# Kernel optimization log

Hardware: AMD Instinct MI355X
Metric: run time of the kernel (lower is better)

Reference implementation:

```python
import jax, jax.numpy as jnp
import numpy as np

D_MODEL = 1024
NUM_HEADS = 16
D_K = D_MODEL // NUM_HEADS


def setup_inputs() -> dict:
    key = jax.random.key(0)
    ks = jax.random.split(key, 7)
    B, S = 2, 2048
    scale = 1.0 / np.sqrt(D_MODEL)
    return {
        "Q": jax.random.normal(ks[0], (B, S, D_MODEL), dtype=jnp.float32),
        "K": jax.random.normal(ks[1], (B, S, D_MODEL), dtype=jnp.float32),
        "V": jax.random.normal(ks[2], (B, S, D_MODEL), dtype=jnp.float32),
        "W_q": jax.random.normal(ks[3], (D_MODEL, D_MODEL), dtype=jnp.float32) * scale,
        "W_k": jax.random.normal(ks[4], (D_MODEL, D_MODEL), dtype=jnp.float32) * scale,
        "W_v": jax.random.normal(ks[5], (D_MODEL, D_MODEL), dtype=jnp.float32) * scale,
        "W_o": jax.random.normal(ks[6], (D_MODEL, D_MODEL), dtype=jnp.float32) * scale,
    }


def _split_heads(x):
    B, S, _ = x.shape
    return x.reshape(B, S, NUM_HEADS, D_K).transpose(0, 2, 1, 3)  # [B,H,S,Dk]


def reference(Q, K, V, W_q, W_k, W_v, W_o):
    # nn.Linear(bias=False): x @ W.T
    q = _split_heads(Q @ W_q.T)
    k = _split_heads(K @ W_k.T)
    v = _split_heads(V @ W_v.T)
    scores = jnp.einsum("bhqd,bhkd->bhqk", q, k) / jnp.sqrt(jnp.float32(D_K))
    probs = jax.nn.softmax(scores, axis=-1)
    out = jnp.einsum("bhqk,bhkd->bhqd", probs, v)  # [B,H,S,Dk]
    B, H, S, Dk = out.shape
    out = out.transpose(0, 2, 1, 3).reshape(B, S, H * Dk)
    return out @ W_o.T
```

## Files before the change

kernel.cpp:

```cpp
#include <hip/hip_runtime.h>
#include <cstdint>

#define D_MODEL 1024
#define NH 16
#define DK 64
#define SEQ 2048
#define BATCH 2
#define M_TOT (BATCH * SEQ)

typedef __bf16 bf16x8          __attribute__((ext_vector_type(8)));
typedef unsigned short u16x8   __attribute__((ext_vector_type(8)));
typedef float  f32x4           __attribute__((ext_vector_type(4)));

union pun8 { u16x8 u; bf16x8 b; };

__device__ __forceinline__ f32x4 mfma16(bf16x8 a, bf16x8 b, f32x4 c) {
    return __builtin_amdgcn_mfma_f32_16x16x32_bf16(a, b, c, 0, 0, 0);
}

__device__ __forceinline__ unsigned short f2bf(float f) {
    union { float f; uint32_t u; } v; v.f = f;
    uint32_t u = v.u;
    return (unsigned short)((u + 0x7FFFu + ((u >> 16) & 1u)) >> 16);
}

__device__ __forceinline__ unsigned short f2bf_trunc(float f) {
    union { float f; uint32_t u; } v; v.f = f;
    return (unsigned short)(v.u >> 16);
}

__device__ __forceinline__ void gl_lds16(const unsigned short* g, unsigned short* l) {
    __builtin_amdgcn_global_load_lds(
        (const __attribute__((address_space(1))) void*)g,
        (__attribute__((address_space(3))) void*)l, 16, 0, 0);
}

#define C_EXP2 0.1803368801111204f

__global__ __launch_bounds__(256) void convert_all_kernel(
    const float* __restrict__ Q,  const float* __restrict__ K,
    const float* __restrict__ V,  const float* __restrict__ Wq,
    const float* __restrict__ Wk, const float* __restrict__ Wv,
    const float* __restrict__ Wo,
    unsigned short* __restrict__ Qb,  unsigned short* __restrict__ Kb,
    unsigned short* __restrict__ Vb,  unsigned short* __restrict__ Wqb,
    unsigned short* __restrict__ Wkb, unsigned short* __restrict__ Wvb,
    unsigned short* __restrict__ Wob)
{
    int bid = blockIdx.x;
    const float* src; unsigned short* dst; int base;
    if (bid < 3 * 2048) {
        int r = bid >> 11;
        src  = (r == 0) ? Q  : (r == 1) ? K  : V;
        dst  = (r == 0) ? Qb : (r == 1) ? Kb : Vb;
        base = (bid & 2047) * 2048;
    } else {
        int u = bid - 3 * 2048;
        int r = u >> 9;
        src  = (r == 0) ? Wq  : (r == 1) ? Wk  : (r == 2) ? Wv  : Wo;
        dst  = (r == 0) ? Wqb : (r == 1) ? Wkb : (r == 2) ? Wvb : Wob;
        base = (u & 511) * 2048;
    }
    int i = base + threadIdx.x * 8;
    float4 a = *(const float4*)(src + i);
    float4 b = *(const float4*)(src + i + 4);
    u16x8 o;
    o[0] = f2bf(a.x); o[1] = f2bf(a.y); o[2] = f2bf(a.z); o[3] = f2bf(a.w);
    o[4] = f2bf(b.x); o[5] = f2bf(b.y); o[6] = f2bf(b.z); o[7] = f2bf(b.w);
    *(u16x8*)(dst + i) = o;
}

__global__ __launch_bounds__(256) void qkv_proj_kernel(
    const unsigned short* __restrict__ Q,
    const unsigned short* __restrict__ K,
    const unsigned short* __restrict__ V,
    const unsigned short* __restrict__ Wq,
    const unsigned short* __restrict__ Wk,
    const unsigned short* __restrict__ Wv,
    unsigned short* __restrict__ qb,
    unsigned short* __restrict__ kb,
    unsigned short* __restrict__ vtb)
{
    const int z = blockIdx.z;
    const unsigned short* A  = (z == 0) ? Q  : (z == 1) ? K  : V;
    const unsigned short* Bt = (z == 0) ? Wq : (z == 1) ? Wk : Wv;

    const int m0 = blockIdx.y * 128;
    const int n0 = blockIdx.x * 128;

    __shared__ __align__(16) unsigned short smem[128 * 136];
    unsigned short* As = smem;
    unsigned short* Bs = smem + 128 * 64;
    unsigned short* Cs = smem;

    const int t    = threadIdx.x;
    const int lane = t & 63;
    const int w    = t >> 6;
    const int l15  = lane & 15;
    const int quad = lane >> 4;
    const int wm   = (w >> 1) * 64;
    const int wn   = (w & 1) * 64;

    f32x4 acc[4][4] = {};

    for (int k0 = 0; k0 < D_MODEL; k0 += 64) {
        __syncthreads();
        #pragma unroll
        for (int i = 0; i < 4; i++) {
            int u   = t + i * 256;
            int row = u >> 3;
            int kc  = (u & 7) * 8;
            gl_lds16(&A [(m0 + row) * D_MODEL + k0 + kc], &As[(i * 256 + w * 64) * 8]);
            gl_lds16(&Bt[(n0 + row) * D_MODEL + k0 + kc], &Bs[(i * 256 + w * 64) * 8]);
        }
        __syncthreads();

        #pragma unroll
        for (int kk = 0; kk < 2; kk++) {
            bf16x8 a[4], b[4];
            #pragma unroll
            for (int mi = 0; mi < 4; mi++)
                a[mi] = *(const bf16x8*)(&As[(wm + mi * 16 + l15) * 64 + kk * 32 + quad * 8]);
            #pragma unroll
            for (int ni = 0; ni < 4; ni++)
                b[ni] = *(const bf16x8*)(&Bs[(wn + ni * 16 + l15) * 64 + kk * 32 + quad * 8]);

            #pragma unroll
            for (int mi = 0; mi < 4; mi++)
                #pragma unroll
                for (int ni = 0; ni < 4; ni++)
                    acc[mi][ni] = mfma16(a[mi], b[ni], acc[mi][ni]);
        }
    }

    const float oscale = (z == 0) ? C_EXP2 : 1.0f;
    __syncthreads();
    #pragma unroll
    for (int mi = 0; mi < 4; mi++) {
        #pragma unroll
        for (int ni = 0; ni < 4; ni++) {
            #pragma unroll
            for (int r = 0; r < 4; r++) {
                int rloc = wm + mi * 16 + quad * 4 + r;
                int cloc = wn + ni * 16 + l15;
                int rr = (z == 2) ? cloc : rloc;
                int cc = (z == 2) ? rloc : cloc;
                Cs[rr * 136 + cc] = f2bf(acc[mi][ni][r] * oscale);
            }
        }
    }
    __syncthreads();
    #pragma unroll
    for (int i = 0; i < 8; i++) {
        int u    = t + i * 256;
        int rrow = u >> 4;
        int cc8  = (u & 15) * 8;
        u16x8 val = *(const u16x8*)(&Cs[rrow * 136 + cc8]);
        unsigned short* dst;
        if (z < 2) {
            int m = m0 + rrow, n = n0 + cc8;
            int bi = m >> 11, s = m & (SEQ - 1);
            int hh = n >> 6,  d = n & (DK - 1);
            dst = ((z == 0) ? qb : kb) + (((size_t)(bi * NH + hh) * SEQ + s) * DK + d);
        } else {
            int dglob = n0 + rrow;
            int bi = m0 >> 11, s = (m0 & (SEQ - 1)) + cc8;
            int hh = dglob >> 6, d = dglob & (DK - 1);
            dst = vtb + (((size_t)(bi * NH + hh) * DK + d) * SEQ + s);
        }
        *(u16x8*)dst = val;
    }
}

__global__ __launch_bounds__(256) void attn_kernel(
    const unsigned short* __restrict__ qb,
    const unsigned short* __restrict__ kb,
    const unsigned short* __restrict__ vtb,
    unsigned short* __restrict__ ctx)
{
    const int h  = blockIdx.x;
    const int qt = blockIdx.y;
    const int b  = blockIdx.z;

    const int t    = threadIdx.x;
    const int lane = t & 63;
    const int w    = t >> 6;
    const int l15  = lane & 15;
    const int quad = lane >> 4;

    const unsigned short* qh = qb  + ((b * NH + h) * SEQ) * DK;
    const unsigned short* kh = kb  + ((b * NH + h) * SEQ) * DK;
    const unsigned short* vh = vtb + ((b * NH + h) * DK) * SEQ;

    __shared__ __align__(16) unsigned short p_lds[4][32][72];
    __shared__ __align__(16) unsigned short Ks[128 * 72];
    __shared__ __align__(16) unsigned short Vs[64 * 136];

    const int qrow0 = qt * 128 + w * 32;
    bf16x8 qa[2][2];
    #pragma unroll
    for (int m = 0; m < 2; m++)
        #pragma unroll
        for (int kk = 0; kk < 2; kk++)
            qa[m][kk] = *(const bf16x8*)(&qh[(qrow0 + m * 16 + l15) * DK + kk * 32 + quad * 8]);

    pun8 ones_p;
    #pragma unroll
    for (int i = 0; i < 8; i++) ones_p.u[i] = 0x3F80;
    const bf16x8 ones = ones_p.b;

    f32x4 o[2][4] = {};
    f32x4 lacc[2] = {};

    for (int kt = 0; kt < SEQ / 128; kt++) {
        __syncthreads();
        #pragma unroll
        for (int i = 0; i < 4; i++) {
            int u   = t + i * 256;
            int row = u >> 3;
            int c8  = (u & 7) * 8;
            *(u16x8*)(&Ks[row * 72 + c8]) =
                *(const u16x8*)(&kh[(kt * 128 + row) * DK + c8]);
        }
        #pragma unroll
        for (int i = 0; i < 4; i++) {
            int u   = t + i * 256;
            int row = u >> 4;
            int c8  = (u & 15) * 8;
            *(u16x8*)(&Vs[row * 136 + c8]) =
                *(const u16x8*)(&vh[row * SEQ + kt * 128 + c8]);
        }
        __syncthreads();

        #pragma unroll
        for (int hh = 0; hh < 2; hh++) {
            bf16x8 kf[4][2], vf[4][2];
            #pragma unroll
            for (int nb = 0; nb < 4; nb++) {
                const int krow = hh * 64 + nb * 16 + l15;
                kf[nb][0] = *(const bf16x8*)(&Ks[krow * 72 + quad * 8]);
                kf[nb][1] = *(const bf16x8*)(&Ks[krow * 72 + 32 + quad * 8]);
            }
            #pragma unroll
            for (int db = 0; db < 4; db++) {
                vf[db][0] = *(const bf16x8*)(&Vs[(db * 16 + l15) * 136 + hh * 64 + quad * 8]);
                vf[db][1] = *(const bf16x8*)(&Vs[(db * 16 + l15) * 136 + hh * 64 + 32 + quad * 8]);
            }

            f32x4 sacc[2][4] = {};
            #pragma unroll
            for (int m = 0; m < 2; m++)
                #pragma unroll
                for (int nb = 0; nb < 4; nb++) {
                    sacc[m][nb] = mfma16(qa[m][0], kf[nb][0], sacc[m][nb]);
                    sacc[m][nb] = mfma16(qa[m][1], kf[nb][1], sacc[m][nb]);
                }

            #pragma unroll
            for (int m = 0; m < 2; m++)
                #pragma unroll
                for (int nb = 0; nb < 4; nb++)
                    #pragma unroll
                    for (int r = 0; r < 4; r++) {
                        float p = exp2f(sacc[m][nb][r]);
                        p_lds[w][m * 16 + quad * 4 + r][nb * 16 + l15] = f2bf_trunc(p);
                    }

            asm volatile("" ::: "memory");

            bf16x8 pa[2][2];
            #pragma unroll
            for (int m = 0; m < 2; m++)
                #pragma unroll
                for (int kk = 0; kk < 2; kk++)
                    pa[m][kk] = *(const bf16x8*)(&p_lds[w][m * 16 + l15][kk * 32 + quad * 8]);

            asm volatile("" ::: "memory");

            #pragma unroll
            for (int db = 0; db < 4; db++)
                #pragma unroll
                for (int m = 0; m < 2; m++) {
                    o[m][db] = mfma16(pa[m][0], vf[db][0], o[m][db]);
                    o[m][db] = mfma16(pa[m][1], vf[db][1], o[m][db]);
                }

            #pragma unroll
            for (int m = 0; m < 2; m++) {
                lacc[m] = mfma16(pa[m][0], ones, lacc[m]);
                lacc[m] = mfma16(pa[m][1], ones, lacc[m]);
            }
        }
    }

    #pragma unroll
    for (int m = 0; m < 2; m++) {
        const int srow_base = b * SEQ + qt * 128 + w * 32 + m * 16 + quad * 4;
        #pragma unroll
        for (int db = 0; db < 4; db++)
            #pragma unroll
            for (int r = 0; r < 4; r++) {
                float val = o[m][db][r] / lacc[m][r];
                ctx[(srow_base + r) * D_MODEL + h * DK + db * 16 + l15] = f2bf(val);
            }
    }
}

__global__ __launch_bounds__(256) void out_proj_kernel(
    const unsigned short* __restrict__ A,
    const unsigned short* __restrict__ Bt,
    float* __restrict__ out)
{
    const int m0 = blockIdx.y * 64;
    const int n0 = blockIdx.x * 128;

    __shared__ __align__(16) unsigned short As[64 * 64];
    __shared__ __align__(16) unsigned short Bs[128 * 64];

    const int t    = threadIdx.x;
    const int lane = t & 63;
    const int w    = t >> 6;
    const int l15  = lane & 15;
    const int quad = lane >> 4;
    const int wn   = w * 32;

    f32x4 acc[4][2] = {};

    for (int k0 = 0; k0 < D_MODEL; k0 += 64) {
        __syncthreads();
        #pragma unroll
        for (int i = 0; i < 2; i++) {
            int u   = t + i * 256;
            int row = u >> 3;
            int kc  = (u & 7) * 8;
            gl_lds16(&A[(m0 + row) * D_MODEL + k0 + kc], &As[(i * 256 + w * 64) * 8]);
        }
        #pragma unroll
        for (int i = 0; i < 4; i++) {
            int u   = t + i * 256;
            int row = u >> 3;
            int kc  = (u & 7) * 8;
            gl_lds16(&Bt[(n0 + row) * D_MODEL + k0 + kc], &Bs[(i * 256 + w * 64) * 8]);
        }
        __syncthreads();

        #pragma unroll
        for (int kk = 0; kk < 2; kk++) {
            bf16x8 a[4], bfr[2];
            #pragma unroll
            for (int mi = 0; mi < 4; mi++)
                a[mi] = *(const bf16x8*)(&As[(mi * 16 + l15) * 64 + kk * 32 + quad * 8]);
            #pragma unroll
            for (int ni = 0; ni < 2; ni++)
                bfr[ni] = *(const bf16x8*)(&Bs[(wn + ni * 16 + l15) * 64 + kk * 32 + quad * 8]);

            #pragma unroll
            for (int mi = 0; mi < 4; mi++)
                #pragma unroll
                for (int ni = 0; ni < 2; ni++)
                    acc[mi][ni] = mfma16(a[mi], bfr[ni], acc[mi][ni]);
        }
    }

    #pragma unroll
    for (int mi = 0; mi < 4; mi++) {
        #pragma unroll
        for (int ni = 0; ni < 2; ni++) {
            #pragma unroll
            for (int r = 0; r < 4; r++) {
                int m = m0 + mi * 16 + quad * 4 + r;
                int n = n0 + wn + ni * 16 + l15;
                out[m * D_MODEL + n] = acc[mi][ni][r];
            }
        }
    }
}

extern "C" void kernel_launch(void* const* d_in, const int* in_sizes, int n_in,
                              void* d_out, int out_size, void* d_ws, size_t ws_size,
                              hipStream_t stream) {
    const float* Q  = (const float*)d_in[0];
    const float* K  = (const float*)d_in[1];
    const float* V  = (const float*)d_in[2];
    const float* Wq = (const float*)d_in[3];
    const float* Wk = (const float*)d_in[4];
    const float* Wv = (const float*)d_in[5];
    const float* Wo = (const float*)d_in[6];

    const size_t NQ = (size_t)M_TOT * D_MODEL;
    const size_t NW = (size_t)D_MODEL * D_MODEL;

    unsigned short* Qb  = (unsigned short*)d_ws;
    unsigned short* Kb  = Qb  + NQ;
    unsigned short* Vb  = Kb  + NQ;
    unsigned short* Wqb = Vb  + NQ;
    unsigned short* Wkb = Wqb + NW;
    unsigned short* Wvb = Wkb + NW;
    unsigned short* Wob = Wvb + NW;
    unsigned short* qb  = Wob + NW;
    unsigned short* kbf = qb  + NQ;
    unsigned short* vtb = kbf + NQ;
    unsigned short* ctx = vtb + NQ;
    float* out = (float*)d_out;

    convert_all_kernel<<<3 * 2048 + 4 * 512, 256, 0, stream>>>(
        Q, K, V, Wq, Wk, Wv, Wo, Qb, Kb, Vb, Wqb, Wkb, Wvb, Wob);

    dim3 g1(D_MODEL / 128, M_TOT / 128, 3);
    qkv_proj_kernel<<<g1, 256, 0, stream>>>(Qb, Kb, Vb, Wqb, Wkb, Wvb, qb, kbf, vtb);

    dim3 g2(NH, SEQ / 128, BATCH);
    attn_kernel<<<g2, 256, 0, stream>>>(qb, kbf, vtb, ctx);

    dim3 g3(D_MODEL / 128, M_TOT / 64, 1);
    out_proj_kernel<<<g3, 256, 0, stream>>>(ctx, Wob, out);
}
```

Baseline: 231.3 us.

## Keep attention probabilities in registers via transposed QK^T and permlane swaps

The attention kernel now computes S^T by swapping MFMA operands, so each lane holds scores along a key row. The probabilities are packed with v_cvt_pk_bf16_f32 and rearranged into the PV A-operand layout with permlane32/permlane16 swaps, which removes the per-wave LDS round-trip buffer for P. It also moves the V fragment loads after the QK^T MFMAs and raises wave priority around the MFMA blocks with s_setprio. This adds gfx950-specific instructions and depends on the lane permutation being exactly right. Rounding also changes from truncation to round-to-nearest.

```diff
diff --git a/kernel.cpp b/kernel.cpp
--- a/kernel.cpp
+++ b/kernel.cpp
@@ -11,6 +11,7 @@
 typedef __bf16 bf16x8          __attribute__((ext_vector_type(8)));
 typedef unsigned short u16x8   __attribute__((ext_vector_type(8)));
 typedef float  f32x4           __attribute__((ext_vector_type(4)));
+typedef unsigned int u32x2     __attribute__((ext_vector_type(2)));
 
 union pun8 { u16x8 u; bf16x8 b; };
 
@@ -24,9 +25,17 @@
     return (unsigned short)((u + 0x7FFFu + ((u >> 16) & 1u)) >> 16);
 }
 
-__device__ __forceinline__ unsigned short f2bf_trunc(float f) {
-    union { float f; uint32_t u; } v; v.f = f;
-    return (unsigned short)(v.u >> 16);
+__device__ __forceinline__ unsigned cvtpk(float lo, float hi) {
+    unsigned r;
+    asm("v_cvt_pk_bf16_f32 %0, %1, %2" : "=v"(r) : "v"(lo), "v"(hi));
+    return r;
+}
+
+__device__ __forceinline__ u32x2 pl32swap(unsigned a, unsigned b) {
+    return __builtin_amdgcn_permlane32_swap(a, b, false, false);
+}
+__device__ __forceinline__ u32x2 pl16swap(unsigned a, unsigned b) {
+    return __builtin_amdgcn_permlane16_swap(a, b, false, false);
 }
 
 __device__ __forceinline__ void gl_lds16(const unsigned short* g, unsigned short* l) {
@@ -192,7 +201,6 @@
     const unsigned short* kh = kb  + ((b * NH + h) * SEQ) * DK;
     const unsigned short* vh = vtb + ((b * NH + h) * DK) * SEQ;
 
-    __shared__ __align__(16) unsigned short p_lds[4][32][72];
     __shared__ __align__(16) unsigned short Ks[128 * 72];
     __shared__ __align__(16) unsigned short Vs[64 * 136];
 
@@ -234,49 +242,60 @@
 
         #pragma unroll
         for (int hh = 0; hh < 2; hh++) {
-            bf16x8 kf[4][2], vf[4][2];
+            bf16x8 kf[4][2];
             #pragma unroll
             for (int nb = 0; nb < 4; nb++) {
                 const int krow = hh * 64 + nb * 16 + l15;
                 kf[nb][0] = *(const bf16x8*)(&Ks[krow * 72 + quad * 8]);
                 kf[nb][1] = *(const bf16x8*)(&Ks[krow * 72 + 32 + quad * 8]);
             }
+
+            f32x4 st[2][4] = {};
+            __builtin_amdgcn_s_setprio(1);
+            #pragma unroll
+            for (int m = 0; m < 2; m++)
+                #pragma unroll
+                for (int nb = 0; nb < 4; nb++) {
+                    st[m][nb] = mfma16(kf[nb][0], qa[m][0], st[m][nb]);
+                    st[m][nb] = mfma16(kf[nb][1], qa[m][1], st[m][nb]);
+                }
+            __builtin_amdgcn_s_setprio(0);
+
+            bf16x8 vf[4][2];
             #pragma unroll
             for (int db = 0; db < 4; db++) {
                 vf[db][0] = *(const bf16x8*)(&Vs[(db * 16 + l15) * 136 + hh * 64 + quad * 8]);
                 vf[db][1] = *(const bf16x8*)(&Vs[(db * 16 + l15) * 136 + hh * 64 + 32 + quad * 8]);
             }
 
-            f32x4 sacc[2][4] = {};
-            #pragma unroll
-            for (int m = 0; m < 2; m++)
+            bf16x8 pa[2][2];
+            #pragma unroll
+            for (int m = 0; m < 2; m++) {
+                unsigned X[4][2];
                 #pragma unroll
                 for (int nb = 0; nb < 4; nb++) {
-                    sacc[m][nb] = mfma16(qa[m][0], kf[nb][0], sacc[m][nb]);
-                    sacc[m][nb] = mfma16(qa[m][1], kf[nb][1], sacc[m][nb]);
+                    float e0 = exp2f(st[m][nb][0]);
+                    float e1 = exp2f(st[m][nb][1]);
+                    float e2 = exp2f(st[m][nb][2]);
+                    float e3 = exp2f(st[m][nb][3]);
+                    X[nb][0] = cvtpk(e0, e1);
+                    X[nb][1] = cvtpk(e2, e3);
                 }
-
-            #pragma unroll
-            for (int m = 0; m < 2; m++)
-                #pragma unroll
-                for (int nb = 0; nb < 4; nb++)
+                #pragma unroll
+                for (int kk = 0; kk < 2; kk++) {
+                    union { unsigned u[4]; bf16x8 b; } wd;
                     #pragma unroll
-                    for (int r = 0; r < 4; r++) {
-                        float p = exp2f(sacc[m][nb][r]);
-                        p_lds[w][m * 16 + quad * 4 + r][nb * 16 + l15] = f2bf_trunc(p);
+                    for (int tt = 0; tt < 2; tt++) {
+                        u32x2 s1 = pl32swap(X[2 * kk][tt], X[2 * kk + 1][tt]);
+                        u32x2 s2 = pl16swap(s1[0], s1[1]);
+                        wd.u[tt]     = s2[0];
+                        wd.u[2 + tt] = s2[1];
                     }
-
-            asm volatile("" ::: "memory");
-
-            bf16x8 pa[2][2];
-            #pragma unroll
-            for (int m = 0; m < 2; m++)
-                #pragma unroll
-                for (int kk = 0; kk < 2; kk++)
-                    pa[m][kk] = *(const bf16x8*)(&p_lds[w][m * 16 + l15][kk * 32 + quad * 8]);
-
-            asm volatile("" ::: "memory");
-
+                    pa[m][kk] = wd.b;
+                }
+            }
+
+            __builtin_amdgcn_s_setprio(1);
             #pragma unroll
             for (int db = 0; db < 4; db++)
                 #pragma unroll
@@ -290,6 +309,7 @@
                 lacc[m] = mfma16(pa[m][0], ones, lacc[m]);
                 lacc[m] = mfma16(pa[m][1], ones, lacc[m]);
             }
+            __builtin_amdgcn_s_setprio(0);
         }
     }
 
```

New measurement: 230.8 us. About the same (-0.2%).

## Split attention query tile over 8 waves and add MFMA priority hints

Applied to the files above, without the earlier changes.

The attention kernel now launches 512 threads per block, with each of 8 waves owning 16 query rows instead of 32. Each wave's per-thread register footprint and the per-thread K/V load work are halved. This is meant to raise occupancy and latency hiding. s_setprio is raised around the MFMA sections so matrix work gets issue priority. The trade-off is that every wave now reloads the same K/V fragments from LDS for half as many rows, which doubles LDS read traffic per useful FLOP.

```diff
diff --git a/kernel.cpp b/kernel.cpp
--- a/kernel.cpp
+++ b/kernel.cpp
@@ -172,7 +172,7 @@
     }
 }
 
-__global__ __launch_bounds__(256) void attn_kernel(
+__global__ __launch_bounds__(512, 4) void attn_kernel(
     const unsigned short* __restrict__ qb,
     const unsigned short* __restrict__ kb,
     const unsigned short* __restrict__ vtb,
@@ -192,39 +192,37 @@
     const unsigned short* kh = kb  + ((b * NH + h) * SEQ) * DK;
     const unsigned short* vh = vtb + ((b * NH + h) * DK) * SEQ;
 
-    __shared__ __align__(16) unsigned short p_lds[4][32][72];
+    __shared__ __align__(16) unsigned short p_lds[8][16][72];
     __shared__ __align__(16) unsigned short Ks[128 * 72];
     __shared__ __align__(16) unsigned short Vs[64 * 136];
 
-    const int qrow0 = qt * 128 + w * 32;
-    bf16x8 qa[2][2];
-    #pragma unroll
-    for (int m = 0; m < 2; m++)
-        #pragma unroll
-        for (int kk = 0; kk < 2; kk++)
-            qa[m][kk] = *(const bf16x8*)(&qh[(qrow0 + m * 16 + l15) * DK + kk * 32 + quad * 8]);
+    const int qrow0 = qt * 128 + w * 16;
+    bf16x8 qa[2];
+    #pragma unroll
+    for (int kk = 0; kk < 2; kk++)
+        qa[kk] = *(const bf16x8*)(&qh[(qrow0 + l15) * DK + kk * 32 + quad * 8]);
 
     pun8 ones_p;
     #pragma unroll
     for (int i = 0; i < 8; i++) ones_p.u[i] = 0x3F80;
     const bf16x8 ones = ones_p.b;
 
-    f32x4 o[2][4] = {};
-    f32x4 lacc[2] = {};
+    f32x4 o[4] = {};
+    f32x4 lacc = {};
 
     for (int kt = 0; kt < SEQ / 128; kt++) {
         __syncthreads();
         #pragma unroll
-        for (int i = 0; i < 4; i++) {
-            int u   = t + i * 256;
+        for (int i = 0; i < 2; i++) {
+            int u   = t + i * 512;
             int row = u >> 3;
             int c8  = (u & 7) * 8;
             *(u16x8*)(&Ks[row * 72 + c8]) =
                 *(const u16x8*)(&kh[(kt * 128 + row) * DK + c8]);
         }
         #pragma unroll
-        for (int i = 0; i < 4; i++) {
-            int u   = t + i * 256;
+        for (int i = 0; i < 2; i++) {
+            int u   = t + i * 512;
             int row = u >> 4;
             int c8  = (u & 15) * 8;
             *(u16x8*)(&Vs[row * 136 + c8]) =
@@ -247,63 +245,52 @@
                 vf[db][1] = *(const bf16x8*)(&Vs[(db * 16 + l15) * 136 + hh * 64 + 32 + quad * 8]);
             }
 
-            f32x4 sacc[2][4] = {};
-            #pragma unroll
-            for (int m = 0; m < 2; m++)
+            f32x4 sacc[4] = {};
+            __builtin_amdgcn_s_setprio(1);
+            #pragma unroll
+            for (int nb = 0; nb < 4; nb++) {
+                sacc[nb] = mfma16(qa[0], kf[nb][0], sacc[nb]);
+                sacc[nb] = mfma16(qa[1], kf[nb][1], sacc[nb]);
+            }
+            __builtin_amdgcn_s_setprio(0);
+
+            #pragma unroll
+            for (int nb = 0; nb < 4; nb++)
                 #pragma unroll
-                for (int nb = 0; nb < 4; nb++) {
-                    sacc[m][nb] = mfma16(qa[m][0], kf[nb][0], sacc[m][nb]);
-                    sacc[m][nb] = mfma16(qa[m][1], kf[nb][1], sacc[m][nb]);
+                for (int r = 0; r < 4; r++) {
+                    float p = exp2f(sacc[nb][r]);
+                    p_lds[w][quad * 4 + r][nb * 16 + l15] = f2bf_trunc(p);
                 }
 
-            #pragma unroll
-            for (int m = 0; m < 2; m++)
-                #pragma unroll
-                for (int nb = 0; nb < 4; nb++)
-                    #pragma unroll
-                    for (int r = 0; r < 4; r++) {
-                        float p = exp2f(sacc[m][nb][r]);
-                        p_lds[w][m * 16 + quad * 4 + r][nb * 16 + l15] = f2bf_trunc(p);
-                    }
-
             asm volatile("" ::: "memory");
 
-            bf16x8 pa[2][2];
-            #pragma unroll
-            for (int m = 0; m < 2; m++)
-                #pragma unroll
-                for (int kk = 0; kk < 2; kk++)
-                    pa[m][kk] = *(const bf16x8*)(&p_lds[w][m * 16 + l15][kk * 32 + quad * 8]);
+            bf16x8 pa[2];
+            #pragma unroll
+            for (int kk = 0; kk < 2; kk++)
+                pa[kk] = *(const bf16x8*)(&p_lds[w][l15][kk * 32 + quad * 8]);
 
             asm volatile("" ::: "memory");
 
-            #pragma unroll
-            for (int db = 0; db < 4; db++)
-                #pragma unroll
-                for (int m = 0; m < 2; m++) {
-                    o[m][db] = mfma16(pa[m][0], vf[db][0], o[m][db]);
-                    o[m][db] = mfma16(pa[m][1], vf[db][1], o[m][db]);
-                }
-
-            #pragma unroll
-            for (int m = 0; m < 2; m++) {
-                lacc[m] = mfma16(pa[m][0], ones, lacc[m]);
-                lacc[m] = mfma16(pa[m][1], ones, lacc[m]);
-            }
-        }
-    }
-
-    #pragma unroll
-    for (int m = 0; m < 2; m++) {
-        const int srow_base = b * SEQ + qt * 128 + w * 32 + m * 16 + quad * 4;
-        #pragma unroll
-        for (int db = 0; db < 4; db++)
-            #pragma unroll
-            for (int r = 0; r < 4; r++) {
-                float val = o[m][db][r] / lacc[m][r];
-                ctx[(srow_base + r) * D_MODEL + h * DK + db * 16 + l15] = f2bf(val);
-            }
-    }
+            __builtin_amdgcn_s_setprio(1);
+            #pragma unroll
+            for (int db = 0; db < 4; db++) {
+                o[db] = mfma16(pa[0], vf[db][0], o[db]);
+                o[db] = mfma16(pa[1], vf[db][1], o[db]);
+            }
+            lacc = mfma16(pa[0], ones, lacc);
+            lacc = mfma16(pa[1], ones, lacc);
+            __builtin_amdgcn_s_setprio(0);
+        }
+    }
+
+    const int srow_base = b * SEQ + qt * 128 + w * 16 + quad * 4;
+    #pragma unroll
+    for (int db = 0; db < 4; db++)
+        #pragma unroll
+        for (int r = 0; r < 4; r++) {
+            float val = o[db][r] / lacc[r];
+            ctx[(srow_base + r) * D_MODEL + h * DK + db * 16 + l15] = f2bf(val);
+        }
 }
 
 __global__ __launch_bounds__(256) void out_proj_kernel(
@@ -410,7 +397,7 @@
     qkv_proj_kernel<<<g1, 256, 0, stream>>>(Qb, Kb, Vb, Wqb, Wkb, Wvb, qb, kbf, vtb);
 
     dim3 g2(NH, SEQ / 128, BATCH);
-    attn_kernel<<<g2, 256, 0, stream>>>(qb, kbf, vtb, ctx);
+    attn_kernel<<<g2, 512, 0, stream>>>(qb, kbf, vtb, ctx);
 
     dim3 g3(D_MODEL / 128, M_TOT / 64, 1);
     out_proj_kernel<<<g3, 256, 0, stream>>>(ctx, Wob, out);
```

New measurement: 235.8 us. About the same (+2.0%).

## Load K/V fragments directly from global memory in attention, use 512-thread blocks

Applied to the files above, without the earlier changes.

The attention kernel stops staging K and V tiles through shared memory and instead loads MFMA fragments straight from global memory (relying on L1/L2 caching), which removes the two __syncthreads per key tile. Blocks grow to 8 waves covering 256 query rows, and s_setprio raises wave priority around the MFMA bursts. This trades LDS traffic and barriers for more redundant global/cache reads, since every wave fetches the same K/V, and the V loads are strided by SEQ.

```diff
diff --git a/kernel.cpp b/kernel.cpp
--- a/kernel.cpp
+++ b/kernel.cpp
@@ -172,7 +172,7 @@
     }
 }
 
-__global__ __launch_bounds__(256) void attn_kernel(
+__global__ __launch_bounds__(512, 2) void attn_kernel(
     const unsigned short* __restrict__ qb,
     const unsigned short* __restrict__ kb,
     const unsigned short* __restrict__ vtb,
@@ -192,11 +192,9 @@
     const unsigned short* kh = kb  + ((b * NH + h) * SEQ) * DK;
     const unsigned short* vh = vtb + ((b * NH + h) * DK) * SEQ;
 
-    __shared__ __align__(16) unsigned short p_lds[4][32][72];
-    __shared__ __align__(16) unsigned short Ks[128 * 72];
-    __shared__ __align__(16) unsigned short Vs[64 * 136];
-
-    const int qrow0 = qt * 128 + w * 32;
+    __shared__ __align__(16) unsigned short p_lds[8][32][72];
+
+    const int qrow0 = qt * 256 + w * 32;
     bf16x8 qa[2][2];
     #pragma unroll
     for (int m = 0; m < 2; m++)
@@ -213,41 +211,20 @@
     f32x4 lacc[2] = {};
 
     for (int kt = 0; kt < SEQ / 128; kt++) {
-        __syncthreads();
-        #pragma unroll
-        for (int i = 0; i < 4; i++) {
-            int u   = t + i * 256;
-            int row = u >> 3;
-            int c8  = (u & 7) * 8;
-            *(u16x8*)(&Ks[row * 72 + c8]) =
-                *(const u16x8*)(&kh[(kt * 128 + row) * DK + c8]);
-        }
-        #pragma unroll
-        for (int i = 0; i < 4; i++) {
-            int u   = t + i * 256;
-            int row = u >> 4;
-            int c8  = (u & 15) * 8;
-            *(u16x8*)(&Vs[row * 136 + c8]) =
-                *(const u16x8*)(&vh[row * SEQ + kt * 128 + c8]);
-        }
-        __syncthreads();
-
         #pragma unroll
         for (int hh = 0; hh < 2; hh++) {
-            bf16x8 kf[4][2], vf[4][2];
+            const int kvbase = kt * 128 + hh * 64;
+
+            bf16x8 kf[4][2];
             #pragma unroll
             for (int nb = 0; nb < 4; nb++) {
-                const int krow = hh * 64 + nb * 16 + l15;
-                kf[nb][0] = *(const bf16x8*)(&Ks[krow * 72 + quad * 8]);
-                kf[nb][1] = *(const bf16x8*)(&Ks[krow * 72 + 32 + quad * 8]);
-            }
-            #pragma unroll
-            for (int db = 0; db < 4; db++) {
-                vf[db][0] = *(const bf16x8*)(&Vs[(db * 16 + l15) * 136 + hh * 64 + quad * 8]);
-                vf[db][1] = *(const bf16x8*)(&Vs[(db * 16 + l15) * 136 + hh * 64 + 32 + quad * 8]);
+                const int krow = kvbase + nb * 16 + l15;
+                kf[nb][0] = *(const bf16x8*)(&kh[krow * DK + quad * 8]);
+                kf[nb][1] = *(const bf16x8*)(&kh[krow * DK + 32 + quad * 8]);
             }
 
             f32x4 sacc[2][4] = {};
+            __builtin_amdgcn_s_setprio(1);
             #pragma unroll
             for (int m = 0; m < 2; m++)
                 #pragma unroll
@@ -255,6 +232,15 @@
                     sacc[m][nb] = mfma16(qa[m][0], kf[nb][0], sacc[m][nb]);
                     sacc[m][nb] = mfma16(qa[m][1], kf[nb][1], sacc[m][nb]);
                 }
+            __builtin_amdgcn_s_setprio(0);
+
+            bf16x8 vf[4][2];
+            #pragma unroll
+            for (int db = 0; db < 4; db++) {
+                const int vrow = (db * 16 + l15) * SEQ + kvbase;
+                vf[db][0] = *(const bf16x8*)(&vh[vrow + quad * 8]);
+                vf[db][1] = *(const bf16x8*)(&vh[vrow + 32 + quad * 8]);
+            }
 
             #pragma unroll
             for (int m = 0; m < 2; m++)
@@ -277,6 +263,7 @@
 
             asm volatile("" ::: "memory");
 
+            __builtin_amdgcn_s_setprio(1);
             #pragma unroll
             for (int db = 0; db < 4; db++)
                 #pragma unroll
@@ -290,12 +277,13 @@
                 lacc[m] = mfma16(pa[m][0], ones, lacc[m]);
                 lacc[m] = mfma16(pa[m][1], ones, lacc[m]);
             }
+            __builtin_amdgcn_s_setprio(0);
         }
     }
 
     #pragma unroll
     for (int m = 0; m < 2; m++) {
-        const int srow_base = b * SEQ + qt * 128 + w * 32 + m * 16 + quad * 4;
+        const int srow_base = b * SEQ + qt * 256 + w * 32 + m * 16 + quad * 4;
         #pragma unroll
         for (int db = 0; db < 4; db++)
             #pragma unroll
@@ -409,8 +397,8 @@
     dim3 g1(D_MODEL / 128, M_TOT / 128, 3);
     qkv_proj_kernel<<<g1, 256, 0, stream>>>(Qb, Kb, Vb, Wqb, Wkb, Wvb, qb, kbf, vtb);
 
-    dim3 g2(NH, SEQ / 128, BATCH);
-    attn_kernel<<<g2, 256, 0, stream>>>(qb, kbf, vtb, ctx);
+    dim3 g2(NH, SEQ / 256, BATCH);
+    attn_kernel<<<g2, 512, 0, stream>>>(qb, kbf, vtb, ctx);
 
     dim3 g3(D_MODEL / 128, M_TOT / 64, 1);
     out_proj_kernel<<<g3, 256, 0, stream>>>(ctx, Wob, out);
```

Result: slower. 282.8 us (+22.3%).
